# Kernel optimization log

Hardware: AMD Instinct MI355X
Metric: run time of the kernel (lower is better)

Reference implementation:

```python
import jax, jax.numpy as jnp
import numpy as np

N0, N1, N2 = 100000, 50000, 50000
E1, E2, E12 = 1600000, 1600000, 800000
D = 128


def scatter_mean(vals, idx, size):
    # torch_scatter.scatter_mean: sum / count, 0 for empty segments
    s = jax.ops.segment_sum(vals, idx, num_segments=size)
    c = jax.ops.segment_sum(jnp.ones((vals.shape[0], 1), vals.dtype), idx, num_segments=size)
    return s / jnp.maximum(c, 1.0)


def setup_inputs() -> dict:
    key = jax.random.key(0)
    ks = jax.random.split(key, 20)
    inp = {
        "x_node": jax.random.normal(ks[0], (N0, D), jnp.float32),
        "x1": jax.random.normal(ks[1], (N1, D), jnp.float32),
        "x2": jax.random.normal(ks[2], (N2, D), jnp.float32),
        "ei1_src": jax.random.randint(ks[3], (E1,), 0, N0, jnp.int32),
        "ei1_dst": jax.random.randint(ks[4], (E1,), 0, N1, jnp.int32),
        "ei2_src": jax.random.randint(ks[5], (E2,), 0, N0, jnp.int32),
        "ei2_dst": jax.random.randint(ks[6], (E2,), 0, N2, jnp.int32),
        "ei12_src": jax.random.randint(ks[7], (E12,), 0, N1, jnp.int32),
        "ei12_dst": jax.random.randint(ks[8], (E12,), 0, N2, jnp.int32),
        "ew1": jax.random.uniform(ks[9], (E1,), jnp.float32),
        "ew2": jax.random.uniform(ks[10], (E2,), jnp.float32),
    }
    # learned params (nn.Linear: y = x @ W.T + b)
    lim = 1.0 / np.sqrt(D)
    inp["W1"] = jax.random.uniform(ks[11], (D, D), jnp.float32, -lim, lim)
    inp["b1"] = jax.random.uniform(ks[12], (D,), jnp.float32, -lim, lim)
    inp["W2"] = jax.random.uniform(ks[13], (D, D), jnp.float32, -lim, lim)
    inp["b2"] = jax.random.uniform(ks[14], (D,), jnp.float32, -lim, lim)
    inp["W12"] = jax.random.uniform(ks[15], (D, D), jnp.float32, -lim, lim)
    inp["b12"] = jax.random.uniform(ks[16], (D,), jnp.float32, -lim, lim)
    xav = np.sqrt(6.0 / (3 + D))
    inp["att_vec"] = jax.random.uniform(ks[17], (3, D), jnp.float32, -xav, xav)
    return inp


def reference(x_node, x1, x2, ei1_src, ei1_dst, ei2_src, ei2_dst,
              ei12_src, ei12_dst, ew1, ew2,
              W1, b1, W2, b2, W12, b12, att_vec):
    n0 = x_node.shape[0]
    # metapath s-1-s
    msg_1 = scatter_mean(x_node[ei1_src] * ew1[:, None], ei1_dst, x1.shape[0])
    net_msg1 = (msg_1 + x1) * 0.5
    s1s = scatter_mean(net_msg1[ei1_dst], ei1_src, n0)
    s1s = jax.nn.relu(s1s @ W1.T + b1)  # dropout: eval mode -> identity

    # metapath s-2-s
    msg_2 = scatter_mean(x_node[ei2_src] * ew2[:, None], ei2_dst, x2.shape[0])
    net_msg2 = (msg_2 + x2) * 0.5
    s2s = scatter_mean(net_msg2[ei2_dst], ei2_src, n0)
    s2s = jax.nn.relu(s2s @ W2.T + b2)

    # metapath s-1-2-s
    msg_1b = scatter_mean(x_node[ei1_src] * ew1[:, None], ei1_dst, x1.shape[0])
    net_1b = (msg_1b + x1) * 0.5
    msg_2b = scatter_mean(net_1b[ei12_src], ei12_dst, x2.shape[0])
    net_2b = (msg_2b + x2) * 0.5
    s12s = scatter_mean(net_2b[ei2_dst] * ew2[:, None], ei2_src, n0)
    s12s = jax.nn.relu(s12s @ W12.T + b12)

    all_mp = jnp.stack([s1s, s2s, s12s], axis=1)  # [N0, 3, D]
    att_scores = jnp.einsum('nkd,kd->nk', all_mp, att_vec)
    att_w = jax.nn.softmax(att_scores, axis=1)
    return jnp.einsum('nkd,nk->nd', all_mp, att_w)
```

## Files before the change

### kernel.cpp

```cpp
#include <hip/hip_runtime.h>
#include <hip/hip_fp16.h>

#define D 128
#define CAP1 80
#define CAP2 56

typedef short s16x8 __attribute__((ext_vector_type(8)));
typedef float f32x4 __attribute__((ext_vector_type(4)));

struct FillJob {
    const int* key;
    const int* other;
    const float* w;
    int* pay;
    int cbase;
    int cap;
    int E, N;
};

__global__ __launch_bounds__(256) void fill_job_kernel(FillJob jb,
                                                       int* __restrict__ cursor) {
    int x = blockIdx.x & 7;
    int gb = blockIdx.x >> 3;
    int lo = (int)((long)jb.N * x / 8);
    int hi = (int)((long)jb.N * (x + 1) / 8);
    bool hasw = (jb.w != nullptr);
    long stride = (long)(gridDim.x >> 3) * 256;
    for (long e = (long)gb * 256 + threadIdx.x; e < jb.E; e += stride) {
        int key = jb.key[e];
        if (key < lo || key >= hi) continue;
        int pos = atomicAdd(&cursor[jb.cbase + key], 1);
        if (pos >= jb.cap) continue;
        int o = jb.other[e];
        int v;
        if (hasw) {
            int w15 = __float2int_rn(jb.w[e] * 32768.0f);
            w15 = w15 > 32767 ? 32767 : w15;
            v = (int)(((unsigned)o << 15) | (unsigned)w15);
        } else {
            v = o;
        }
        jb.pay[(long)key * jb.cap + pos] = v;
    }
}

__global__ void f2h_kernel(const float2* __restrict__ in, __half2* __restrict__ o,
                           long n2) {
    long i = (long)blockIdx.x * blockDim.x + threadIdx.x;
    if (i < n2) o[i] = __float22half2_rn(in[i]);
}

__global__ void wsplit_kernel(const float* __restrict__ W1,
                              const float* __restrict__ W2,
                              const float* __restrict__ W12,
                              unsigned short* __restrict__ hi,
                              unsigned short* __restrict__ lo) {
    int i = blockIdx.x * 256 + threadIdx.x;
    if (i >= 3 * D * D) return;
    int p = i >> 14, r = i & (D * D - 1);
    const float* W = p == 0 ? W1 : (p == 1 ? W2 : W12);
    float x = W[r];
    unsigned u = __float_as_uint(x);
    unsigned hb = u & 0xFFFF0000u;
    hi[i] = (unsigned short)(hb >> 16);
    float rem = x - __uint_as_float(hb);
    lo[i] = (unsigned short)(__float_as_uint(rem) >> 16);
}

__device__ __forceinline__ void acc8(float4 raw, float mul, float2 a[4]) {
    const __half2* h = (const __half2*)&raw;
#pragma unroll
    for (int k = 0; k < 4; ++k) {
        float2 f = __half22float2(h[k]);
        a[k].x = fmaf(f.x, mul, a[k].x);
        a[k].y = fmaf(f.y, mul, a[k].y);
    }
}

template <bool HASW>
__global__ __launch_bounds__(256) void aggh_kernel(
    const __half* __restrict__ vals, int vstride, const int* __restrict__ cnt,
    int cap, const int* __restrict__ pay, const float* __restrict__ xb,
    __half* __restrict__ dst, int dstride, int doff, int N) {
    int node = (int)(((long)blockIdx.x * 256 + threadIdx.x) >> 6);
    int lane = threadIdx.x & 63;
    if (node >= N) return;
    int count = cnt[node];
    int m = count < cap ? count : cap;
    long b0 = (long)node * cap;
    int grp = lane >> 4, il = lane & 15;
    float2 a[4] = {{0.f, 0.f}, {0.f, 0.f}, {0.f, 0.f}, {0.f, 0.f}};
    for (int base = 0; base < m; base += 64) {
        int rem = m - base;
        int n = rem < 64 ? rem : 64;
        int p = 0;
        if (lane < n) p = pay[b0 + base + lane];
        for (int j = 0; j < n; j += 4) {
            int jj = j + grp;
            int pj = __shfl(p, jj, 64);
            int g;
            float wt;
            if (HASW) {
                g = (int)(((unsigned)pj) >> 15);
                wt = (float)(pj & 0x7fff) * (1.0f / 32768.0f);
            } else {
                g = pj;
                wt = 1.0f;
            }
            float mul = jj < n ? wt : 0.0f;
            float4 raw = ((const float4*)(vals + (long)g * vstride))[il];
            acc8(raw, mul, a);
        }
    }
#pragma unroll
    for (int k = 0; k < 4; ++k) {
        a[k].x += __shfl_xor(a[k].x, 16, 64);
        a[k].y += __shfl_xor(a[k].y, 16, 64);
        a[k].x += __shfl_xor(a[k].x, 32, 64);
        a[k].y += __shfl_xor(a[k].y, 32, 64);
    }
    if (lane < 16) {
        float inv = 1.0f / fmaxf((float)count, 1.0f);
        const float4* xp = (const float4*)(xb + (long)node * D + il * 8);
        float4 x0 = xp[0], x1 = xp[1];
        float rx[8] = {x0.x, x0.y, x0.z, x0.w, x1.x, x1.y, x1.z, x1.w};
        __half2 h[4];
#pragma unroll
        for (int k = 0; k < 4; ++k) {
            float2 r;
            r.x = (a[k].x * inv + rx[2 * k + 0]) * 0.5f;
            r.y = (a[k].y * inv + rx[2 * k + 1]) * 0.5f;
            h[k] = __float22half2_rn(r);
        }
        *(float4*)(dst + (long)node * dstride + doff + il * 8) = *(float4*)h;
    }
}

__global__ __launch_bounds__(256) void aggf_kernel(
    const __half* __restrict__ vals, const int* __restrict__ cnt, int cap,
    const int* __restrict__ pay, float* __restrict__ out, int N) {
    int node = (int)(((long)blockIdx.x * 256 + threadIdx.x) >> 6);
    int lane = threadIdx.x & 63;
    if (node >= N) return;
    int count = cnt[node];
    int m = count < cap ? count : cap;
    long b0 = (long)node * cap;
    int grp = lane >> 4, il = lane & 15;
    float2 a[4] = {{0.f, 0.f}, {0.f, 0.f}, {0.f, 0.f}, {0.f, 0.f}};
    for (int base = 0; base < m; base += 64) {
        int rem = m - base;
        int n = rem < 64 ? rem : 64;
        int p = 0;
        if (lane < n) p = pay[b0 + base + lane];
        for (int j = 0; j < n; j += 4) {
            int jj = j + grp;
            int pj = __shfl(p, jj, 64);
            float mul = jj < n ? 1.0f : 0.0f;
            float4 raw = ((const float4*)(vals + (long)pj * D))[il];
            acc8(raw, mul, a);
        }
    }
#pragma unroll
    for (int k = 0; k < 4; ++k) {
        a[k].x += __shfl_xor(a[k].x, 16, 64);
        a[k].y += __shfl_xor(a[k].y, 16, 64);
        a[k].x += __shfl_xor(a[k].x, 32, 64);
        a[k].y += __shfl_xor(a[k].y, 32, 64);
    }
    if (lane < 16) {
        float inv = 1.0f / fmaxf((float)count, 1.0f);
        float4* op = (float4*)(out + (long)node * D + il * 8);
        float4 o0 = {a[0].x * inv, a[0].y * inv, a[1].x * inv, a[1].y * inv};
        float4 o1 = {a[2].x * inv, a[2].y * inv, a[3].x * inv, a[3].y * inv};
        op[0] = o0;
        op[1] = o1;
    }
}

__global__ __launch_bounds__(256) void agg2_kernel(
    const __half* __restrict__ combo, const int* __restrict__ cnt, int cap,
    const int* __restrict__ pay, float* __restrict__ outa,
    float* __restrict__ outb, int N) {
    int node = (int)(((long)blockIdx.x * 256 + threadIdx.x) >> 6);
    int lane = threadIdx.x & 63;
    if (node >= N) return;
    int count = cnt[node];
    int m = count < cap ? count : cap;
    long b0 = (long)node * cap;
    int grp = lane >> 5, il = lane & 31;
    float2 a[4] = {{0.f, 0.f}, {0.f, 0.f}, {0.f, 0.f}, {0.f, 0.f}};
    int p = 0;
    if (lane < m) p = pay[b0 + lane];
    for (int j = 0; j < m; j += 2) {
        int jj = j + grp;
        int pj = __shfl(p, jj, 64);
        int g = (int)(((unsigned)pj) >> 15);
        float w = (float)(pj & 0x7fff) * (1.0f / 32768.0f);
        float mul = jj < m ? (il < 16 ? 1.0f : w) : 0.0f;
        float4 raw = ((const float4*)(combo + (long)g * 256))[il];
        acc8(raw, mul, a);
    }
#pragma unroll
    for (int k = 0; k < 4; ++k) {
        a[k].x += __shfl_xor(a[k].x, 32, 64);
        a[k].y += __shfl_xor(a[k].y, 32, 64);
    }
    if (lane < 32) {
        float inv = 1.0f / fmaxf((float)count, 1.0f);
        float* o = (il < 16) ? (outa + (long)node * D + il * 8)
                             : (outb + (long)node * D + (il - 16) * 8);
        float4 o0 = {a[0].x * inv, a[0].y * inv, a[1].x * inv, a[1].y * inv};
        float4 o1 = {a[2].x * inv, a[2].y * inv, a[3].x * inv, a[3].y * inv};
        ((float4*)o)[0] = o0;
        ((float4*)o)[1] = o1;
    }
}

__global__ __launch_bounds__(256) void mfma_tail_kernel(
    const float* __restrict__ pre1, const float* __restrict__ pre2,
    const float* pre3, const unsigned short* __restrict__ Whi,
    const unsigned short* __restrict__ Wlo, const float* __restrict__ b1,
    const float* __restrict__ b2, const float* __restrict__ b12,
    const float* __restrict__ att, float* out, int N) {
    int wv = (int)(((long)blockIdx.x * 256 + threadIdx.x) >> 6);
    int lane = threadIdx.x & 63;
    int m0 = wv * 16;
    if (m0 >= N) return;
    int rw = lane & 15;
    int kg = lane >> 4;
    int mrow = m0 + rw;
    if (mrow >= N) mrow = N - 1;
    const float* PRE[3] = {pre1, pre2, pre3};
    const float* BB[3] = {b1, b2, b12};

    f32x4 acc[3][8];
#pragma unroll
    for (int p = 0; p < 3; ++p)
#pragma unroll
        for (int c = 0; c < 8; ++c) acc[p][c] = (f32x4){0.f, 0.f, 0.f, 0.f};

#pragma unroll
    for (int p = 0; p < 3; ++p) {
        const float* src = PRE[p] + (long)mrow * D + kg * 8;
        const unsigned short* whp = Whi + ((long)p << 14) + rw * D + kg * 8;
        const unsigned short* wlp = Wlo + ((long)p << 14) + rw * D + kg * 8;
#pragma unroll
        for (int kt = 0; kt < 4; ++kt) {
            float4 xa = *(const float4*)(src + kt * 32);
            float4 xb = *(const float4*)(src + kt * 32 + 4);
            float xs[8] = {xa.x, xa.y, xa.z, xa.w, xb.x, xb.y, xb.z, xb.w};
            s16x8 ah, al;
#pragma unroll
            for (int i = 0; i < 8; ++i) {
                unsigned u = __float_as_uint(xs[i]);
                unsigned hb = u & 0xFFFF0000u;
                ah[i] = (short)(hb >> 16);
                float rem = xs[i] - __uint_as_float(hb);
                al[i] = (short)(__float_as_uint(rem) >> 16);
            }
#pragma unroll
            for (int c = 0; c < 8; ++c) {
                s16x8 bh = *(const s16x8*)(whp + c * (16 * D) + kt * 32);
                s16x8 bl = *(const s16x8*)(wlp + c * (16 * D) + kt * 32);
                acc[p][c] = __builtin_amdgcn_mfma_f32_16x16x32_bf16(
                    ah, bh, acc[p][c], 0, 0, 0);
                acc[p][c] = __builtin_amdgcn_mfma_f32_16x16x32_bf16(
                    ah, bl, acc[p][c], 0, 0, 0);
                acc[p][c] = __builtin_amdgcn_mfma_f32_16x16x32_bf16(
                    al, bh, acc[p][c], 0, 0, 0);
            }
        }
    }

    float sc[3][4] = {{0.f, 0.f, 0.f, 0.f},
                      {0.f, 0.f, 0.f, 0.f},
                      {0.f, 0.f, 0.f, 0.f}};
#pragma unroll
    for (int p = 0; p < 3; ++p) {
#pragma unroll
        for (int c = 0; c < 8; ++c) {
            float bv = BB[p][c * 16 + rw];
            float av = att[p * D + c * 16 + rw];
#pragma unroll
            for (int j = 0; j < 4; ++j) {
                float v = fmaxf(acc[p][c][j] + bv, 0.0f);
                acc[p][c][j] = v;
                sc[p][j] = fmaf(v, av, sc[p][j]);
            }
        }
    }
#pragma unroll
    for (int j = 0; j < 4; ++j) {
#pragma unroll
        for (int off = 1; off < 16; off <<= 1) {
            sc[0][j] += __shfl_xor(sc[0][j], off, 64);
            sc[1][j] += __shfl_xor(sc[1][j], off, 64);
            sc[2][j] += __shfl_xor(sc[2][j], off, 64);
        }
    }
#pragma unroll
    for (int j = 0; j < 4; ++j) {
        float s0 = sc[0][j], s1 = sc[1][j], s2 = sc[2][j];
        float mx = fmaxf(s0, fmaxf(s1, s2));
        float e0 = __expf(s0 - mx), e1 = __expf(s1 - mx), e2 = __expf(s2 - mx);
        float inv = 1.0f / (e0 + e1 + e2);
        float w0 = e0 * inv, w1 = e1 * inv, w2 = e2 * inv;
        int orow = m0 + kg * 4 + j;
        if (orow < N) {
            long ro = (long)orow * D + rw;
#pragma unroll
            for (int c = 0; c < 8; ++c) {
                out[ro + c * 16] =
                    acc[0][c][j] * w0 + acc[1][c][j] * w1 + acc[2][c][j] * w2;
            }
        }
    }
}

extern "C" void kernel_launch(void* const* d_in, const int* in_sizes, int n_in,
                              void* d_out, int out_size, void* d_ws,
                              size_t ws_size, hipStream_t stream) {
    const float* x_node = (const float*)d_in[0];
    const float* x1 = (const float*)d_in[1];
    const float* x2 = (const float*)d_in[2];
    const int* ei1_src = (const int*)d_in[3];
    const int* ei1_dst = (const int*)d_in[4];
    const int* ei2_src = (const int*)d_in[5];
    const int* ei2_dst = (const int*)d_in[6];
    const int* ei12_src = (const int*)d_in[7];
    const int* ei12_dst = (const int*)d_in[8];
    const float* ew1 = (const float*)d_in[9];
    const float* ew2 = (const float*)d_in[10];
    const float* W1 = (const float*)d_in[11];
    const float* b1 = (const float*)d_in[12];
    const float* W2 = (const float*)d_in[13];
    const float* b2 = (const float*)d_in[14];
    const float* W12 = (const float*)d_in[15];
    const float* b12 = (const float*)d_in[16];
    const float* att = (const float*)d_in[17];
    float* out = (float*)d_out;

    const int N0 = in_sizes[0] / D;
    const int N1 = in_sizes[1] / D;
    const int N2 = in_sizes[2] / D;
    const int E1 = in_sizes[3];
    const int E2 = in_sizes[5];
    const int E12 = in_sizes[7];

    float* ws = (float*)d_ws;
    size_t off = 0;
    auto A = [](size_t v) { return (v + 3) & ~(size_t)3; };

    __half* xh = (__half*)(ws + off);    off += A((size_t)N0 * D / 2);
    __half* net1h = (__half*)(ws + off); off += A((size_t)N1 * D / 2);
    __half* combo = (__half*)(ws + off); off += A((size_t)N2 * D);

    size_t pA = off;
    int* pay_d12 = (int*)(ws + off); off += A((size_t)N2 * CAP2);
    int* pay_s1 = (int*)(ws + off);  off += A((size_t)N0 * CAP2);
    size_t needA = pA + (size_t)N0 * D;
    if (off < needA) off = needA;
    float* pre2 = ws + pA;

    size_t pB = off;
    int* pay_d1 = (int*)(ws + off); off += A((size_t)N1 * CAP1);
    int* pay_d2 = (int*)(ws + off); off += A((size_t)N2 * CAP1);
    size_t needB = pB + (size_t)N0 * D;
    if (off < needB) off = needB;
    float* pre1 = ws + pB;

    int* pay_s2 = (int*)(ws + off); off += A((size_t)N0 * CAP2);
    float* pre3 = out;

    unsigned short* Whi = (unsigned short*)(ws + off); off += A((size_t)3 * D * D / 2);
    unsigned short* Wlo = (unsigned short*)(ws + off); off += A((size_t)3 * D * D / 2);

    const int NT = N1 + 2 * N2 + 2 * N0;
    int* cur = (int*)(ws + off); off += A(NT);
    const int cb_d1 = 0, cb_d2 = N1, cb_d12 = N1 + N2;
    const int cb_s1 = N1 + 2 * N2, cb_s2 = N1 + 2 * N2 + N0;

    hipMemsetAsync((void*)cur, 0, (size_t)NT * sizeof(int), stream);

    long n2 = (long)N0 * D / 2;
    f2h_kernel<<<(n2 + 255) / 256, 256, 0, stream>>>((const float2*)x_node,
                                                     (__half2*)xh, n2);
    wsplit_kernel<<<(3 * D * D + 255) / 256, 256, 0, stream>>>(W1, W2, W12,
                                                               Whi, Wlo);

    FillJob F[5] = {
        {ei1_dst, ei1_src, ew1, pay_d1, cb_d1, CAP1, E1, N1},
        {ei2_dst, ei2_src, ew2, pay_d2, cb_d2, CAP1, E2, N2},
        {ei12_dst, ei12_src, nullptr, pay_d12, cb_d12, CAP2, E12, N2},
        {ei1_src, ei1_dst, nullptr, pay_s1, cb_s1, CAP2, E1, N0},
        {ei2_src, ei2_dst, ew2, pay_s2, cb_s2, CAP2, E2, N0},
    };
    for (int j = 0; j < 5; ++j)
        fill_job_kernel<<<2048, 256, 0, stream>>>(F[j], cur);

    auto blocks = [](int n) { return (n + 3) / 4; };
    aggh_kernel<true><<<blocks(N1), 256, 0, stream>>>(
        xh, D, cur + cb_d1, CAP1, pay_d1, x1, net1h, D, 0, N1);
    aggh_kernel<true><<<blocks(N2), 256, 0, stream>>>(
        xh, D, cur + cb_d2, CAP1, pay_d2, x2, combo, 2 * D, 0, N2);
    aggh_kernel<false><<<blocks(N2), 256, 0, stream>>>(
        net1h, D, cur + cb_d12, CAP2, pay_d12, x2, combo, 2 * D, D, N2);
    aggf_kernel<<<blocks(N0), 256, 0, stream>>>(net1h, cur + cb_s1, CAP2,
                                                pay_s1, pre1, N0);
    agg2_kernel<<<blocks(N0), 256, 0, stream>>>(combo, cur + cb_s2, CAP2,
                                                pay_s2, pre2, pre3, N0);

    const int nwaves = (N0 + 15) / 16;
    mfma_tail_kernel<<<(nwaves + 3) / 4, 256, 0, stream>>>(
        pre1, pre2, pre3, Whi, Wlo, b1, b2, b12, att, out, N0);
}
```

Measured before the change: 1.011 ms.

## Split tail MFMA output columns across two waves with shared-memory score reduction

The tail kernel now has two waves share each 16-row strip, each wave computing half of the 128 output columns. This halves the accumulator registers per wave, and launch bounds request higher occupancy. The partial attention scores from the two halves are combined through shared memory behind a block barrier. The cost is that each wave reloads and re-splits the input rows redundantly, and the kernel gains a __syncthreads.

```diff
diff --git a/kernel.cpp b/kernel.cpp
--- a/kernel.cpp
+++ b/kernel.cpp
@@ -216,34 +216,36 @@
     }
 }
 
-__global__ __launch_bounds__(256) void mfma_tail_kernel(
+__global__ __launch_bounds__(256, 4) void mfma_tail_kernel(
     const float* __restrict__ pre1, const float* __restrict__ pre2,
     const float* pre3, const unsigned short* __restrict__ Whi,
     const unsigned short* __restrict__ Wlo, const float* __restrict__ b1,
     const float* __restrict__ b2, const float* __restrict__ b12,
     const float* __restrict__ att, float* out, int N) {
-    int wv = (int)(((long)blockIdx.x * 256 + threadIdx.x) >> 6);
-    int lane = threadIdx.x & 63;
-    int m0 = wv * 16;
-    if (m0 >= N) return;
-    int rw = lane & 15;
-    int kg = lane >> 4;
+    __shared__ float sred[2][2][3][16];
+    int tid = threadIdx.x;
+    int w = tid >> 6, lane = tid & 63;
+    int strip = w >> 1, half = w & 1;
+    int rw = lane & 15, kg = lane >> 4;
+    int m0 = blockIdx.x * 32 + strip * 16;
     int mrow = m0 + rw;
     if (mrow >= N) mrow = N - 1;
     const float* PRE[3] = {pre1, pre2, pre3};
     const float* BB[3] = {b1, b2, b12};
 
-    f32x4 acc[3][8];
+    f32x4 acc[3][4];
 #pragma unroll
     for (int p = 0; p < 3; ++p)
 #pragma unroll
-        for (int c = 0; c < 8; ++c) acc[p][c] = (f32x4){0.f, 0.f, 0.f, 0.f};
+        for (int c = 0; c < 4; ++c) acc[p][c] = (f32x4){0.f, 0.f, 0.f, 0.f};
 
 #pragma unroll
     for (int p = 0; p < 3; ++p) {
         const float* src = PRE[p] + (long)mrow * D + kg * 8;
-        const unsigned short* whp = Whi + ((long)p << 14) + rw * D + kg * 8;
-        const unsigned short* wlp = Wlo + ((long)p << 14) + rw * D + kg * 8;
+        const unsigned short* whp =
+            Whi + ((long)p << 14) + (long)(half * 64 + rw) * D + kg * 8;
+        const unsigned short* wlp =
+            Wlo + ((long)p << 14) + (long)(half * 64 + rw) * D + kg * 8;
 #pragma unroll
         for (int kt = 0; kt < 4; ++kt) {
             float4 xa = *(const float4*)(src + kt * 32);
@@ -259,7 +261,7 @@
                 al[i] = (short)(__float_as_uint(rem) >> 16);
             }
 #pragma unroll
-            for (int c = 0; c < 8; ++c) {
+            for (int c = 0; c < 4; ++c) {
                 s16x8 bh = *(const s16x8*)(whp + c * (16 * D) + kt * 32);
                 s16x8 bl = *(const s16x8*)(wlp + c * (16 * D) + kt * 32);
                 acc[p][c] = __builtin_amdgcn_mfma_f32_16x16x32_bf16(
@@ -278,9 +280,10 @@
 #pragma unroll
     for (int p = 0; p < 3; ++p) {
 #pragma unroll
-        for (int c = 0; c < 8; ++c) {
-            float bv = BB[p][c * 16 + rw];
-            float av = att[p * D + c * 16 + rw];
+        for (int c = 0; c < 4; ++c) {
+            int col = half * 64 + c * 16 + rw;
+            float bv = BB[p][col];
+            float av = att[p * D + col];
 #pragma unroll
             for (int j = 0; j < 4; ++j) {
                 float v = fmaxf(acc[p][c][j] + bv, 0.0f);
@@ -298,18 +301,30 @@
             sc[2][j] += __shfl_xor(sc[2][j], off, 64);
         }
     }
+    if (rw == 0) {
+#pragma unroll
+        for (int p = 0; p < 3; ++p)
+#pragma unroll
+            for (int j = 0; j < 4; ++j)
+                sred[strip][half][p][kg * 4 + j] = sc[p][j];
+    }
+    __syncthreads();
+
 #pragma unroll
     for (int j = 0; j < 4; ++j) {
-        float s0 = sc[0][j], s1 = sc[1][j], s2 = sc[2][j];
+        int row = kg * 4 + j;
+        float s0 = sred[strip][0][0][row] + sred[strip][1][0][row];
+        float s1 = sred[strip][0][1][row] + sred[strip][1][1][row];
+        float s2 = sred[strip][0][2][row] + sred[strip][1][2][row];
         float mx = fmaxf(s0, fmaxf(s1, s2));
         float e0 = __expf(s0 - mx), e1 = __expf(s1 - mx), e2 = __expf(s2 - mx);
         float inv = 1.0f / (e0 + e1 + e2);
         float w0 = e0 * inv, w1 = e1 * inv, w2 = e2 * inv;
-        int orow = m0 + kg * 4 + j;
+        int orow = m0 + row;
         if (orow < N) {
-            long ro = (long)orow * D + rw;
-#pragma unroll
-            for (int c = 0; c < 8; ++c) {
+            long ro = (long)orow * D + half * 64 + rw;
+#pragma unroll
+            for (int c = 0; c < 4; ++c) {
                 out[ro + c * 16] =
                     acc[0][c][j] * w0 + acc[1][c][j] * w1 + acc[2][c][j] * w2;
             }
@@ -410,7 +425,6 @@
     agg2_kernel<<<blocks(N0), 256, 0, stream>>>(combo, cur + cb_s2, CAP2,
                                                 pay_s2, pre2, pre3, N0);
 
-    const int nwaves = (N0 + 15) / 16;
-    mfma_tail_kernel<<<(nwaves + 3) / 4, 256, 0, stream>>>(
+    mfma_tail_kernel<<<(N0 + 31) / 32, 256, 0, stream>>>(
         pre1, pre2, pre3, Whi, Wlo, b1, b2, b12, att, out, N0);
 }
```

After: 1.016 ms. Within noise of the previous version (+0.5%).
